# Kernel tuning notes

Measured on AMD Instinct MI355X. Metric: run time of the kernel, lower is better.

## Reference

```python
import jax, jax.numpy as jnp
import numpy as np

NUM_HEADS = 16
HEAD_DIM = 128
EMBED = NUM_HEADS * HEAD_DIM  # 2048
BATCH, SEQ = 2, 2048


def setup_inputs() -> dict:
    key = jax.random.key(0)
    k1, k2 = jax.random.split(key)
    x = jax.random.normal(k1, (BATCH, SEQ, EMBED), dtype=jnp.float32)
    W = jax.random.normal(k2, (EMBED, 3 * EMBED), dtype=jnp.float32) * 0.02
    b = jnp.zeros((3 * EMBED,), dtype=jnp.float32)
    return {"x": x, "W": W, "b": b}


def _rotate_half(u):
    u1, u2 = jnp.split(u, 2, axis=-1)
    return jnp.concatenate([-u2, u1], axis=-1)


def reference(x, W, b):
    B, S, E = x.shape
    H, D = NUM_HEADS, HEAD_DIM
    # Fused QKV projection: [B,S,E] @ [E,3E] -> [B,S,3E]
    qkv = jnp.einsum('bse,ef->bsf', x, W) + b
    qkv = qkv.reshape(B, S, 3, H, D)
    q, k, v = qkv[:, :, 0], qkv[:, :, 1], qkv[:, :, 2]  # each [B,S,H,D]
    # Module's rotary embedding: sin/cos over arange(S*D), shared across heads
    t = jnp.arange(S * D, dtype=jnp.float32).reshape(1, S, 1, D)
    sin, cos = jnp.sin(t), jnp.cos(t)
    q = q * cos + _rotate_half(q) * sin
    k = k * cos + _rotate_half(k) * sin
    # Scaled dot-product attention over sequence, per head
    scale = 1.0 / jnp.sqrt(jnp.float32(D))
    attn = jnp.einsum('bqhd,bkhd->bhqk', q, k) * scale  # [B,H,S,S]
    w = jax.nn.softmax(attn, axis=-1)
    out = jnp.einsum('bhqk,bkhd->bqhd', w, v)  # [B,S,H,D]
    return out
```

## Files before the change

kernel.cpp:

```cpp
#include <hip/hip_runtime.h>
#include <stdint.h>

typedef unsigned short u16;
typedef __attribute__((ext_vector_type(8))) short bf16x8;
typedef __attribute__((ext_vector_type(4))) float f32x4;

#define NUM_B 2
#define SEQ   2048
#define SEQP  2080
#define NH    16
#define HD    128
#define EMB   2048
#define N3    6144
#define MM    4096
#define QT    64
#define WQ    32
#define KT    32
#define NTILE (SEQ / KT)

#define BM 128
#define BN 384
#define BK 64
#define NT_K (EMB / BK)

__device__ __forceinline__ u16 f2bf(float f) {
  union { float f; unsigned u; } c; c.f = f;
  return (u16)((c.u + 0x7FFFu + ((c.u >> 16) & 1u)) >> 16);
}
__device__ __forceinline__ void async16(const void* g, void* l) {
  __builtin_amdgcn_global_load_lds(
      (const __attribute__((address_space(1))) void*)g,
      (__attribute__((address_space(3))) void*)l, 16, 0, 0);
}

#define GBAR()   asm volatile("s_barrier" ::: "memory")
#define WLGKM0() asm volatile("s_waitcnt lgkmcnt(0)" ::: "memory")


__global__ void k_cvt_bf16(const float* __restrict__ in, u16* __restrict__ out,
                           float2* __restrict__ tab, int n4) {
  int i = blockIdx.x * blockDim.x + threadIdx.x;
  if (i >= n4) return;
  const float4 v = ((const float4*)in)[i];
  ushort4 o;
  o.x = f2bf(v.x); o.y = f2bf(v.y); o.z = f2bf(v.z); o.w = f2bf(v.w);
  ((ushort4*)out)[i] = o;
  if (i < SEQ * HD) {
    double t = (double)i;
    tab[i] = make_float2((float)cos(t), (float)sin(t));
  }
}

__global__ void k_transpose_w(const float* __restrict__ W, u16* __restrict__ Wt) {
  __shared__ float t[32][33];
  int n0 = blockIdx.x * 32, k0 = blockIdx.y * 32;
  int tx = threadIdx.x, ty = threadIdx.y;
  #pragma unroll
  for (int i = ty; i < 32; i += 8)
    t[i][tx] = W[(size_t)(k0 + i) * N3 + n0 + tx];
  __syncthreads();
  #pragma unroll
  for (int i = ty; i < 32; i += 8)
    Wt[(size_t)(n0 + i) * EMB + k0 + tx] = f2bf(t[tx][i]);
}

__global__ __launch_bounds__(512, 2) void k_gemm_qkv(
    const u16* __restrict__ xb, const u16* __restrict__ wt,
    const float* __restrict__ bias, const float2* __restrict__ tab,
    u16* __restrict__ qb, u16* __restrict__ kb, u16* __restrict__ vbt)
{
  __shared__ __align__(16) u16 lsA[2][BM * BK];
  __shared__ __align__(16) u16 lsB[2][BN * BK];
  const int tid = threadIdx.x;
  const int wave = tid >> 6, lane = tid & 63;
  const int lq = lane & 15, lr = lane >> 4;
  const int wr = wave >> 2, wc = wave & 3;
  const int m0 = blockIdx.y * BM, n0 = blockIdx.x * BN;

  auto stA = [&](int t) {
    const int kt = t * BK;
    #pragma unroll
    for (int ii = 0; ii < 2; ++ii) {
      int s = ii * 512 + tid;
      int row = s >> 3, gq = (s & 7) ^ (row & 7);
      async16(xb + (size_t)(m0 + row) * EMB + kt + gq * 8, &lsA[t & 1][s * 8]);
    }
  };
  auto stB = [&](int t, int u) {
    const int kt = t * BK;
    #pragma unroll
    for (int ii = 0; ii < 2; ++ii) {
      int s = u * 1024 + ii * 512 + tid;
      int row = s >> 3, gq = (s & 7) ^ (row & 7);
      async16(wt + (size_t)(n0 + row) * EMB + kt + gq * 8, &lsB[t & 1][s * 8]);
    }
  };

  f32x4 acc[4][6];
  #pragma unroll
  for (int i = 0; i < 4; ++i)
    #pragma unroll
    for (int j = 0; j < 6; ++j)
      acc[i][j] = f32x4{0.f, 0.f, 0.f, 0.f};

  int rbase[6];
  #pragma unroll
  for (int nf = 0; nf < 6; ++nf) {
    int pg = 3 * wc + (nf >> 1);
    int col = (pg >> 2) * 128 + (pg & 3) * 16 + (nf & 1) * 64 + lq;
    rbase[nf] = col * BK;
  }
  const int aRow0 = (wr * 64 + lq) * BK;
  int qsw[2];
  qsw[0] = ((0 + lr) ^ (lq & 7)) * 8;
  qsw[1] = ((4 + lr) ^ (lq & 7)) * 8;

  stA(0); stB(0, 0); stB(0, 1); stB(0, 2); stB(1, 0); stB(1, 1); stB(1, 2);
  asm volatile("s_waitcnt vmcnt(6)" ::: "memory");
  GBAR();

  for (int ti = 0; ti < NT_K / 2; ++ti) {
    const int t0 = 2 * ti, t1 = t0 + 1;
    const bool nl = (ti < NT_K / 2 - 1);

    #pragma unroll
    for (int hp = 0; hp < 2; ++hp) {
      const u16* Ap = lsA[hp];
      const u16* Bp = lsB[hp];
      bf16x8 bfr[6][2];

      #pragma unroll
      for (int ph = 0; ph < 2; ++ph) {
        if (ph == 0) {
          #pragma unroll
          for (int nf = 0; nf < 6; ++nf)
            #pragma unroll
            for (int kk = 0; kk < 2; ++kk)
              bfr[nf][kk] = *(const bf16x8*)(Bp + rbase[nf] + qsw[kk]);
        }
        bf16x8 af[2][2];
        #pragma unroll
        for (int mfl = 0; mfl < 2; ++mfl)
          #pragma unroll
          for (int kk = 0; kk < 2; ++kk)
            af[mfl][kk] = *(const bf16x8*)(Ap + aRow0 + ((ph * 2 + mfl) * 16) * BK + qsw[kk]);

        if (hp == 0) {
          if (ph == 0) {
            stA(t1);
          } else {
            if (nl) {
              stB(t0 + 2, 0); stB(t0 + 2, 1);
              asm volatile("s_waitcnt vmcnt(4)" ::: "memory");
            } else {
              asm volatile("s_waitcnt vmcnt(0)" ::: "memory");
            }
          }
        } else {
          if (ph == 0) {
            if (nl) { stA(t0 + 2); stB(t0 + 2, 2); }
          } else {
            if (nl) {
              stB(t1 + 2, 0); stB(t1 + 2, 1); stB(t1 + 2, 2);
              asm volatile("s_waitcnt vmcnt(6)" ::: "memory");
            }
          }
        }
        if (ph == 0) asm volatile("s_waitcnt lgkmcnt(8)" ::: "memory");

        GBAR();
        WLGKM0();
        __builtin_amdgcn_s_setprio(1);
        #pragma unroll
        for (int kk = 0; kk < 2; ++kk)
          #pragma unroll
          for (int mfl = 0; mfl < 2; ++mfl)
            #pragma unroll
            for (int nf = 0; nf < 6; ++nf)
              acc[ph * 2 + mfl][nf] = __builtin_amdgcn_mfma_f32_16x16x32_bf16(
                  af[mfl][kk], bfr[nf][kk], acc[ph * 2 + mfl][nf], 0, 0, 0);
        __builtin_amdgcn_s_setprio(0);
        GBAR();
      }
    }
  }

  const int m0w = m0 + wr * 64;
  const int bxH = n0 >> 7;
  #pragma unroll
  for (int pl = 0; pl < 3; ++pl) {
    const int pg = 3 * wc + pl;
    const int j = pg >> 2;
    const int s4 = pg & 3;
    const int H = bxH + j;
    const int w = H >> 4;
    const int h = H & 15;
    const int d1 = s4 * 16 + lq;
    const float b1 = bias[n0 + j * 128 + d1];
    const float b2 = bias[n0 + j * 128 + d1 + 64];

    if (w == 2) {
      #pragma unroll
      for (int mf = 0; mf < 4; ++mf) {
        int mg0 = m0w + mf * 16 + lr * 4;
        int b = mg0 >> 11, s0 = mg0 & 2047;
        ushort4 pk;
        pk.x = f2bf(acc[mf][2 * pl][0] + b1);
        pk.y = f2bf(acc[mf][2 * pl][1] + b1);
        pk.z = f2bf(acc[mf][2 * pl][2] + b1);
        pk.w = f2bf(acc[mf][2 * pl][3] + b1);
        *(ushort4*)(vbt + ((size_t)(b * NH + h) * HD + d1) * SEQP + s0) = pk;
        pk.x = f2bf(acc[mf][2 * pl + 1][0] + b2);
        pk.y = f2bf(acc[mf][2 * pl + 1][1] + b2);
        pk.z = f2bf(acc[mf][2 * pl + 1][2] + b2);
        pk.w = f2bf(acc[mf][2 * pl + 1][3] + b2);
        *(ushort4*)(vbt + ((size_t)(b * NH + h) * HD + d1 + 64) * SEQP + s0) = pk;
      }
    } else {
      u16* basep = (w == 0) ? qb : kb;
      const float qs = (w == 0) ? 0.12751569843736827f : 1.0f;
      #pragma unroll
      for (int mf = 0; mf < 4; ++mf)
        #pragma unroll
        for (int r = 0; r < 4; ++r) {
          int mg = m0w + mf * 16 + lr * 4 + r;
          int b = mg >> 11, s = mg & 2047;
          u16* dst = basep + ((size_t)(b * NH + h) * SEQ + s) * HD;
          float c1 = acc[mf][2 * pl][r]     + b1;
          float c2 = acc[mf][2 * pl + 1][r] + b2;
          float2 s1 = tab[s * HD + d1];
          float2 s2 = tab[s * HD + d1 + 64];
          dst[d1]      = f2bf((c1 * s1.x - c2 * s1.y) * qs);
          dst[d1 + 64] = f2bf((c2 * s2.x + c1 * s2.y) * qs);
        }
    }
  }
}

__global__ __launch_bounds__(128, 2) void k_flash(
    const u16* __restrict__ qb, const u16* __restrict__ kb,
    const u16* __restrict__ vbt, float* __restrict__ out)
{
  __shared__ __align__(16) u16 lsK[2][KT * HD];
  __shared__ __align__(16) u16 lsV[2][HD * KT];
  __shared__ __align__(16) u16 lsP[2][WQ * KT];

  const int tid = threadIdx.x;
  const int wave = tid >> 6, lane = tid & 63;
  const int lq = lane & 15, lr = lane >> 4;
  const int i = blockIdx.x;
  const int xcd = i & 7, j = i >> 3;
  const int bh = xcd * 4 + (j >> 5);
  const int q0 = (j & 31) * QT;
  const u16* Qg = qb + ((size_t)bh * SEQ + q0 + wave * WQ) * HD;
  const u16* Kg = kb + (size_t)bh * SEQ * HD;
  const u16* Vg = vbt + (size_t)bh * HD * SEQP;

  auto stage = [&](int tile, int buf) {
    const int k0 = tile * KT;
    #pragma unroll
    for (int ii = 0; ii < 4; ++ii) {
      int c = tid + ii * 128;
      int key = c >> 4, grp = c & 15;
      async16(Kg + (size_t)(k0 + key) * HD + ((grp ^ (key & 7)) * 8), lsK[buf] + c * 8);
    }
    #pragma unroll
    for (int ii = 0; ii < 4; ++ii) {
      int c = tid + ii * 128;
      int d = c >> 2, g2 = c & 3;
      async16(Vg + (size_t)d * SEQP + k0 + ((g2 ^ ((d >> 1) & 3)) * 8), lsV[buf] + c * 8);
    }
  };

  stage(0, 0);

  bf16x8 qf[2][4];
  #pragma unroll
  for (int qq = 0; qq < 2; ++qq)
    #pragma unroll
    for (int ks = 0; ks < 4; ++ks)
      qf[qq][ks] = *(const bf16x8*)(Qg + (size_t)(qq * 16 + lq) * HD + ks * 32 + lr * 8);

  f32x4 acc_o[2][8];
  float lsum[2] = {0.f, 0.f};
  #pragma unroll
  for (int mb = 0; mb < 2; ++mb)
    #pragma unroll
    for (int nb = 0; nb < 8; ++nb) acc_o[mb][nb] = f32x4{0.f, 0.f, 0.f, 0.f};

  for (int t = 0; t < NTILE; ++t) {
    const int p = t & 1;
    __syncthreads();
    if (t + 1 < NTILE) stage(t + 1, 1 - p);

    f32x4 sacc[2][2];
    #pragma unroll
    for (int kbi = 0; kbi < 2; ++kbi)
      #pragma unroll
      for (int qq = 0; qq < 2; ++qq) sacc[kbi][qq] = f32x4{0.f, 0.f, 0.f, 0.f};
    __builtin_amdgcn_s_setprio(1);
    #pragma unroll
    for (int ks = 0; ks < 4; ++ks) {
      bf16x8 kf[2];
      #pragma unroll
      for (int kbi = 0; kbi < 2; ++kbi) {
        int key = kbi * 16 + lq;
        int g = (ks * 4 + lr) ^ (key & 7);
        kf[kbi] = *(const bf16x8*)(lsK[p] + key * HD + g * 8);
      }
      #pragma unroll
      for (int kbi = 0; kbi < 2; ++kbi)
        #pragma unroll
        for (int qq = 0; qq < 2; ++qq)
          sacc[kbi][qq] = __builtin_amdgcn_mfma_f32_16x16x32_bf16(kf[kbi], qf[qq][ks], sacc[kbi][qq], 0, 0, 0);
    }
    __builtin_amdgcn_s_setprio(0);

    #pragma unroll
    for (int kbi = 0; kbi < 2; ++kbi)
      #pragma unroll
      for (int qq = 0; qq < 2; ++qq) {
        float p0 = __builtin_amdgcn_exp2f(sacc[kbi][qq][0]);
        float p1 = __builtin_amdgcn_exp2f(sacc[kbi][qq][1]);
        float p2 = __builtin_amdgcn_exp2f(sacc[kbi][qq][2]);
        float p3 = __builtin_amdgcn_exp2f(sacc[kbi][qq][3]);
        lsum[qq] += (p0 + p1) + (p2 + p3);
        int row = qq * 16 + lq;
        int g = kbi * 4 + lr;
        int gp = g ^ (row & 6);
        uint2 pk;
        pk.x = (uint32_t)f2bf(p0) | ((uint32_t)f2bf(p1) << 16);
        pk.y = (uint32_t)f2bf(p2) | ((uint32_t)f2bf(p3) << 16);
        *(uint2*)(lsP[wave] + row * KT + gp * 4) = pk;
      }

    bf16x8 ap[2];
    #pragma unroll
    for (int mb = 0; mb < 2; ++mb) {
      int row = mb * 16 + lq;
      int gp = (2 * lr) ^ (row & 6);
      ap[mb] = *(const bf16x8*)(lsP[wave] + row * KT + gp * 4);
    }
    __builtin_amdgcn_s_setprio(1);
    #pragma unroll
    for (int nb = 0; nb < 8; ++nb) {
      int d = nb * 16 + lq;
      int g2 = lr ^ ((d >> 1) & 3);
      bf16x8 bv = *(const bf16x8*)(lsV[p] + d * KT + g2 * 8);
      #pragma unroll
      for (int mb = 0; mb < 2; ++mb)
        acc_o[mb][nb] = __builtin_amdgcn_mfma_f32_16x16x32_bf16(ap[mb], bv[0] == bv[0] ? bv : bv, acc_o[mb][nb], 0, 0, 0);
    }
    __builtin_amdgcn_s_setprio(0);
  }

  float inv[2];
  #pragma unroll
  for (int qq = 0; qq < 2; ++qq) {
    float s = lsum[qq];
    s += __shfl_xor(s, 16);
    s += __shfl_xor(s, 32);
    inv[qq] = 1.0f / s;
  }
  const int b = bh >> 4, h = bh & 15;
  #pragma unroll
  for (int mb = 0; mb < 2; ++mb)
    #pragma unroll
    for (int r = 0; r < 4; ++r) {
      float iv = __shfl(inv[mb], lr * 4 + r);
      int row = wave * WQ + mb * 16 + lr * 4 + r;
      int sq = q0 + row;
      float* op = out + (((size_t)b * SEQ + sq) * NH + h) * HD;
      #pragma unroll
      for (int nb = 0; nb < 8; ++nb)
        op[nb * 16 + lq] = acc_o[mb][nb][r] * iv;
    }
}


extern "C" void kernel_launch(void* const* d_in, const int* in_sizes, int n_in,
                              void* d_out, int out_size, void* d_ws, size_t ws_size,
                              hipStream_t stream) {
  (void)in_sizes; (void)n_in; (void)out_size; (void)ws_size;
  const float* x    = (const float*)d_in[0];
  const float* W    = (const float*)d_in[1];
  const float* bias = (const float*)d_in[2];
  float* out = (float*)d_out;

  char* p = (char*)d_ws;
  u16* xb  = (u16*)p;  p += (size_t)MM * EMB * 2;
  u16* wt  = (u16*)p;  p += (size_t)N3 * EMB * 2;
  u16* qb  = (u16*)p;  p += (size_t)NUM_B * NH * SEQ * HD * 2;
  u16* kb  = (u16*)p;  p += (size_t)NUM_B * NH * SEQ * HD * 2;
  u16* vbt = (u16*)p;  p += (size_t)NUM_B * NH * HD * SEQP * 2;
  float2* tab = (float2*)p;

  k_cvt_bf16<<<(MM * EMB / 4 + 255) / 256, 256, 0, stream>>>(x, xb, tab, MM * EMB / 4);
  k_transpose_w<<<dim3(N3 / 32, EMB / 32), dim3(32, 8), 0, stream>>>(W, wt);
  k_gemm_qkv<<<dim3(N3 / BN, MM / BM), 512, 0, stream>>>(xb, wt, bias, tab, qb, kb, vbt);
  k_flash<<<SEQ / QT * NUM_B * NH, 128, 0, stream>>>(qb, kb, vbt, out);
}
```

Measured before the change: 237.8 us.

## Widen flash blocks to 8 waves sharing K/V tiles and fuse prep kernels

The flash attention kernel now handles 256 query rows per block with 8 waves instead of 64 rows with 2 waves. Each staged K/V tile is therefore reused by four times as many waves, cutting redundant global loads, and each thread issues one async load per tile instead of four. The bf16 conversion and weight transpose kernels are merged into one launch to remove a kernel boundary. In exchange the grid shrinks to 256 blocks at one block per CU, which may reduce latency hiding and leave some CUs idle.

```diff
diff --git a/kernel.cpp b/kernel.cpp
--- a/kernel.cpp
+++ b/kernel.cpp
@@ -13,7 +13,7 @@
 #define EMB   2048
 #define N3    6144
 #define MM    4096
-#define QT    64
+#define QT    256
 #define WQ    32
 #define KT    32
 #define NTILE (SEQ / KT)
@@ -36,32 +36,35 @@
 #define GBAR()   asm volatile("s_barrier" ::: "memory")
 #define WLGKM0() asm volatile("s_waitcnt lgkmcnt(0)" ::: "memory")
 
-
-__global__ void k_cvt_bf16(const float* __restrict__ in, u16* __restrict__ out,
-                           float2* __restrict__ tab, int n4) {
-  int i = blockIdx.x * blockDim.x + threadIdx.x;
-  if (i >= n4) return;
-  const float4 v = ((const float4*)in)[i];
-  ushort4 o;
-  o.x = f2bf(v.x); o.y = f2bf(v.y); o.z = f2bf(v.z); o.w = f2bf(v.w);
-  ((ushort4*)out)[i] = o;
-  if (i < SEQ * HD) {
-    double t = (double)i;
-    tab[i] = make_float2((float)cos(t), (float)sin(t));
-  }
-}
-
-__global__ void k_transpose_w(const float* __restrict__ W, u16* __restrict__ Wt) {
+#define CVT_BLKS (MM * EMB / 4 / 256)
+#define TRN_BX   (N3 / 32)
+__global__ void k_prep(const float* __restrict__ x, u16* __restrict__ xb,
+                       float2* __restrict__ tab,
+                       const float* __restrict__ W, u16* __restrict__ Wt) {
   __shared__ float t[32][33];
-  int n0 = blockIdx.x * 32, k0 = blockIdx.y * 32;
-  int tx = threadIdx.x, ty = threadIdx.y;
-  #pragma unroll
-  for (int i = ty; i < 32; i += 8)
-    t[i][tx] = W[(size_t)(k0 + i) * N3 + n0 + tx];
-  __syncthreads();
-  #pragma unroll
-  for (int i = ty; i < 32; i += 8)
-    Wt[(size_t)(n0 + i) * EMB + k0 + tx] = f2bf(t[tx][i]);
+  const int bid = blockIdx.x;
+  if (bid < CVT_BLKS) {
+    int i = bid * 256 + threadIdx.x;
+    const float4 v = ((const float4*)x)[i];
+    ushort4 o;
+    o.x = f2bf(v.x); o.y = f2bf(v.y); o.z = f2bf(v.z); o.w = f2bf(v.w);
+    ((ushort4*)xb)[i] = o;
+    if (i < SEQ * HD) {
+      double tt = (double)i;
+      tab[i] = make_float2((float)cos(tt), (float)sin(tt));
+    }
+  } else {
+    int b2 = bid - CVT_BLKS;
+    int n0 = (b2 % TRN_BX) * 32, k0 = (b2 / TRN_BX) * 32;
+    int tx = threadIdx.x & 31, ty = threadIdx.x >> 5;
+    #pragma unroll
+    for (int i = ty; i < 32; i += 8)
+      t[i][tx] = W[(size_t)(k0 + i) * N3 + n0 + tx];
+    __syncthreads();
+    #pragma unroll
+    for (int i = ty; i < 32; i += 8)
+      Wt[(size_t)(n0 + i) * EMB + k0 + tx] = f2bf(t[tx][i]);
+  }
 }
 
 __global__ __launch_bounds__(512, 2) void k_gemm_qkv(
@@ -237,36 +240,34 @@
   }
 }
 
-__global__ __launch_bounds__(128, 2) void k_flash(
+__global__ __launch_bounds__(512, 1) void k_flash(
     const u16* __restrict__ qb, const u16* __restrict__ kb,
     const u16* __restrict__ vbt, float* __restrict__ out)
 {
   __shared__ __align__(16) u16 lsK[2][KT * HD];
   __shared__ __align__(16) u16 lsV[2][HD * KT];
-  __shared__ __align__(16) u16 lsP[2][WQ * KT];
+  __shared__ __align__(16) u16 lsP[8][WQ * KT];
 
   const int tid = threadIdx.x;
   const int wave = tid >> 6, lane = tid & 63;
   const int lq = lane & 15, lr = lane >> 4;
   const int i = blockIdx.x;
   const int xcd = i & 7, j = i >> 3;
-  const int bh = xcd * 4 + (j >> 5);
-  const int q0 = (j & 31) * QT;
+  const int bh = xcd * 4 + (j >> 3);
+  const int q0 = (j & 7) * QT;
   const u16* Qg = qb + ((size_t)bh * SEQ + q0 + wave * WQ) * HD;
   const u16* Kg = kb + (size_t)bh * SEQ * HD;
   const u16* Vg = vbt + (size_t)bh * HD * SEQP;
 
   auto stage = [&](int tile, int buf) {
     const int k0 = tile * KT;
-    #pragma unroll
-    for (int ii = 0; ii < 4; ++ii) {
-      int c = tid + ii * 128;
+    {
+      int c = tid;
       int key = c >> 4, grp = c & 15;
       async16(Kg + (size_t)(k0 + key) * HD + ((grp ^ (key & 7)) * 8), lsK[buf] + c * 8);
     }
-    #pragma unroll
-    for (int ii = 0; ii < 4; ++ii) {
-      int c = tid + ii * 128;
+    {
+      int c = tid;
       int d = c >> 2, g2 = c & 3;
       async16(Vg + (size_t)d * SEQP + k0 + ((g2 ^ ((d >> 1) & 3)) * 8), lsV[buf] + c * 8);
     }
@@ -395,8 +396,7 @@
   u16* vbt = (u16*)p;  p += (size_t)NUM_B * NH * HD * SEQP * 2;
   float2* tab = (float2*)p;
 
-  k_cvt_bf16<<<(MM * EMB / 4 + 255) / 256, 256, 0, stream>>>(x, xb, tab, MM * EMB / 4);
-  k_transpose_w<<<dim3(N3 / 32, EMB / 32), dim3(32, 8), 0, stream>>>(W, wt);
+  k_prep<<<CVT_BLKS + TRN_BX * (EMB / 32), 256, 0, stream>>>(x, xb, tab, W, wt);
   k_gemm_qkv<<<dim3(N3 / BN, MM / BM), 512, 0, stream>>>(xb, wt, bias, tab, qb, kb, vbt);
-  k_flash<<<SEQ / QT * NUM_B * NH, 128, 0, stream>>>(qb, kb, vbt, out);
-}
+  k_flash<<<SEQ / QT * NUM_B * NH, 512, 0, stream>>>(qb, kb, vbt, out);
+}
```

Measured after the change: 230.6 us. 3.0% less time.
